# Kernel optimization log

Hardware: AMD Instinct MI355X
Metric: run time of the kernel (lower is better)

Reference implementation:

```python
import jax, jax.numpy as jnp
import numpy as np

EMB = 768
HEADS = 8

def setup_inputs() -> dict:
    key = jax.random.key(0)
    ks = jax.random.split(key, 9)
    B, N, E = 16, 1024, EMB
    s = 1.0 / np.sqrt(E)
    x = jax.random.normal(ks[0], (B, N, E), dtype=jnp.float32)
    Wq = jax.random.normal(ks[1], (E, E), dtype=jnp.float32) * s
    bq = jnp.zeros((E,), dtype=jnp.float32)
    Wk = jax.random.normal(ks[2], (E, E), dtype=jnp.float32) * s
    bk = jnp.zeros((E,), dtype=jnp.float32)
    Wv = jax.random.normal(ks[3], (E, E), dtype=jnp.float32) * s
    bv = jnp.zeros((E,), dtype=jnp.float32)
    Wo = jax.random.normal(ks[4], (E, E), dtype=jnp.float32) * s
    bo = jnp.zeros((E,), dtype=jnp.float32)
    return {"x": x, "Wq": Wq, "bq": bq, "Wk": Wk, "bk": bk, "Wv": Wv, "bv": bv, "Wo": Wo, "bo": bo}

def reference(x, Wq, bq, Wk, bk, Wv, bv, Wo, bo):
    B, N, E = x.shape
    H = HEADS
    D = E // H
    # separate Q/K/V linears, split heads: b n (h d) -> b h n d
    q = (x @ Wq + bq).reshape(B, N, H, D).transpose(0, 2, 1, 3)
    k = (x @ Wk + bk).reshape(B, N, H, D).transpose(0, 2, 1, 3)
    v = (x @ Wv + bv).reshape(B, N, H, D).transpose(0, 2, 1, 3)
    energy = jnp.einsum('bhqd,bhkd->bhqk', q, k)
    # NON-STANDARD: softmax first, then divide by sqrt(emb_size)
    scaling = jnp.float32(E) ** 0.5
    attn = jax.nn.softmax(energy, axis=-1) / scaling
    out = jnp.einsum('bhqk,bhkd->bhqd', attn, v)
    out = out.transpose(0, 2, 1, 3).reshape(B, N, E)  # b h n d -> b n (h d)
    return out @ Wo + bo
```

## Files before the change

### kernel.cpp

```cpp
#include <hip/hip_runtime.h>


typedef _Float16 half8 __attribute__((ext_vector_type(8)));
typedef __fp16 fp16x2 __attribute__((ext_vector_type(2)));
typedef float f32x4 __attribute__((ext_vector_type(4)));
typedef float f32x16 __attribute__((ext_vector_type(16)));

__device__ __forceinline__ void gload_lds16(const void* g, void* l) {
  __builtin_amdgcn_global_load_lds((const __attribute__((address_space(1))) void*)g,
                                   (__attribute__((address_space(3))) void*)l, 16, 0, 0);
}


__global__ __launch_bounds__(256) void conv_x_kernel(const float* __restrict__ x,
                                                     _Float16* __restrict__ xh) {
  long i = ((long)blockIdx.x * 256 + threadIdx.x) * 8;
  float4 a = *(const float4*)(x + i);
  float4 b = *(const float4*)(x + i + 4);
  half8 o;
  o[0] = (_Float16)a.x; o[1] = (_Float16)a.y; o[2] = (_Float16)a.z; o[3] = (_Float16)a.w;
  o[4] = (_Float16)b.x; o[5] = (_Float16)b.y; o[6] = (_Float16)b.z; o[7] = (_Float16)b.w;
  *(half8*)(xh + i) = o;
}

__global__ __launch_bounds__(256) void transpose_cvt_kernel(
    const float* __restrict__ W0, const float* __restrict__ W1,
    const float* __restrict__ W2, const float* __restrict__ W3,
    _Float16* __restrict__ WT) {
  __shared__ float tile[32][33];
  int z = blockIdx.z;
  const float* W = (z == 0) ? W0 : (z == 1) ? W1 : (z == 2) ? W2 : W3;
  int k0 = blockIdx.y * 32, n0 = blockIdx.x * 32;
  int tx = threadIdx.x, ty = threadIdx.y;
#pragma unroll
  for (int j = ty; j < 32; j += 8)
    tile[j][tx] = W[(size_t)(k0 + j) * 768 + n0 + tx];
  __syncthreads();
  _Float16* dst = WT + (size_t)z * 768 * 768;
#pragma unroll
  for (int j = ty; j < 32; j += 8)
    dst[(size_t)(n0 + j) * 768 + k0 + tx] = (_Float16)tile[tx][j];
}

__global__ __launch_bounds__(256) void conv_bias_kernel(const float* __restrict__ bq,
                                                        const float* __restrict__ bk,
                                                        const float* __restrict__ bv,
                                                        float* __restrict__ bias) {
  int i = blockIdx.x * 256 + threadIdx.x;
  if (i >= 2304) return;
  bias[i] = (i < 768) ? bq[i] : (i < 1536) ? bk[i - 768] : bv[i - 1536];
}


template <int OUT_F16>
__global__ __launch_bounds__(512, 2) void gemm256_kernel(
    const _Float16* __restrict__ A, const _Float16* __restrict__ Bt,
    const float* __restrict__ bias, void* __restrict__ C,
    int M, int N, int K, int ldc) {
  __shared__ _Float16 As[2][256 * 64];
  __shared__ _Float16 Bs[2][256 * 64];
  int nbx = N >> 8;
  int nwg = gridDim.x, wg = blockIdx.x;
  int cpx = nwg >> 3;
  int swz = (wg & 7) * cpx + (wg >> 3);
  int bx = swz % nbx, by = swz / nbx;
  int m0 = by * 256, n0 = bx * 256;
  int t = threadIdx.x, l = t & 63, w = t >> 6;
  int lg = l >> 4, lr = l & 15;
  int wr = w >> 2, wc = w & 3;
  f32x4 acc[8][4] = {};

  int srow[4], ssc[4];
#pragma unroll
  for (int j = 0; j < 4; ++j) {
    int slot = j * 512 + t;
    srow[j] = slot >> 3;
    ssc[j] = ((slot & 7) ^ (srow[j] & 7)) * 8;
  }

  auto stage = [&](int kt, int bi) {
    int k0 = kt * 64;
#pragma unroll
    for (int j = 0; j < 4; ++j)
      gload_lds16(A + (size_t)(m0 + srow[j]) * K + k0 + ssc[j], &As[bi][(j * 512 + t) * 8]);
#pragma unroll
    for (int j = 0; j < 4; ++j)
      gload_lds16(Bt + (size_t)(n0 + srow[j]) * K + k0 + ssc[j], &Bs[bi][(j * 512 + t) * 8]);
  };

  auto compute = [&](int bi) {
#pragma unroll
    for (int kk = 0; kk < 2; ++kk) {
      half8 bf[4];
#pragma unroll
      for (int nf = 0; nf < 4; ++nf) {
        int row = wc * 64 + nf * 16 + lr;
        bf[nf] = *(const half8*)&Bs[bi][row * 64 + ((kk * 4 + lg) ^ (row & 7)) * 8];
      }
#pragma unroll
      for (int mf = 0; mf < 8; ++mf) {
        int row = wr * 128 + mf * 16 + lr;
        half8 af = *(const half8*)&As[bi][row * 64 + ((kk * 4 + lg) ^ (row & 7)) * 8];
#pragma unroll
        for (int nf = 0; nf < 4; ++nf)
          acc[mf][nf] = __builtin_amdgcn_mfma_f32_16x16x32_f16(af, bf[nf], acc[mf][nf], 0, 0, 0);
      }
    }
  };

  int nkt = K >> 6;
  stage(0, 0);
  for (int kt = 0; kt < nkt; ++kt) {
    int bi = kt & 1;
    if (kt + 1 < nkt) {
      stage(kt + 1, bi ^ 1);
      asm volatile("s_waitcnt vmcnt(8)" ::: "memory");
    } else {
      asm volatile("s_waitcnt vmcnt(0)" ::: "memory");
    }
    __builtin_amdgcn_sched_barrier(0);
    __builtin_amdgcn_s_barrier();
    __builtin_amdgcn_sched_barrier(0);
    compute(bi);
    __builtin_amdgcn_sched_barrier(0);
    __builtin_amdgcn_s_barrier();
  }

#pragma unroll
  for (int mf = 0; mf < 8; ++mf)
#pragma unroll
    for (int nf = 0; nf < 4; ++nf) {
      int col = n0 + wc * 64 + nf * 16 + lr;
      float bb = bias[col];
#pragma unroll
      for (int i = 0; i < 4; ++i) {
        int row = m0 + wr * 128 + mf * 16 + lg * 4 + i;
        float v = acc[mf][nf][i] + bb;
        if (OUT_F16)
          ((_Float16*)C)[(size_t)row * ldc + col] = (_Float16)v;
        else
          ((float*)C)[(size_t)row * ldc + col] = v;
      }
    }
}


__global__ __launch_bounds__(256, 2) void attn_kernel(const _Float16* __restrict__ QKV,
                                                      _Float16* __restrict__ Oh) {
  int hw = blockIdx.x;
  int lin = (hw & 7) * 128 + (hw >> 3);
  int bh = lin >> 3, qt = lin & 7;
  int b = bh >> 3, h = bh & 7;
  int t = threadIdx.x, w = t >> 6, l = t & 63;
  int lr = l & 31, hi = l >> 5;

  __shared__ __align__(16) char KF[2][12288];
  __shared__ __align__(16) _Float16 VF[2][96 * 64];

  const _Float16* Qb = QKV + (size_t)b * 1024 * 2304 + h * 96;
  const _Float16* Kb = Qb + 768;
  const _Float16* Vb = Qb + 1536;

  half8 qf[6];
  {
    int qrow = qt * 128 + w * 32 + lr;
    const _Float16 s = (_Float16)1.4426950408889634f;
#pragma unroll
    for (int c = 0; c < 6; ++c) {
      qf[c] = *(const half8*)&Qb[(size_t)qrow * 2304 + c * 16 + hi * 8];
#pragma unroll
      for (int e = 0; e < 8; ++e) qf[c][e] = qf[c][e] * s;
    }
  }

  int ks_src[3], ks_dst[3];
#pragma unroll
  for (int j = 0; j < 3; ++j) {
    int s = j * 256 + t;
    int f = s >> 6, lane = s & 63;
    int sb = f / 6, c = f - sb * 6;
    ks_src[j] = (sb * 32 + (lane & 31)) * 2304 + c * 16 + ((lane >> 5) & 1) * 8;
    ks_dst[j] = s * 16;
  }
  bool vact[2];
  int v_src[2], v_dst[2][8];
#pragma unroll
  for (int j = 0; j < 2; ++j) {
    int u = j * 256 + t;
    vact[j] = u < 384;
    int kvp = u / 12, mm = u % 12;
    v_src[j] = 2 * kvp * 2304 + mm * 8;
#pragma unroll
    for (int e = 0; e < 8; ++e) {
      int d = mm * 8 + e;
      int sw = ((d & 7) ^ ((d >> 3) & 7)) << 3;
      v_dst[j][e] = d * 64 + ((2 * kvp) ^ sw);
    }
  }

  auto stage = [&](int kv0, int bi) {
    size_t goff = (size_t)kv0 * 2304;
#pragma unroll
    for (int j = 0; j < 3; ++j)
      gload_lds16(Kb + goff + ks_src[j], &KF[bi][ks_dst[j]]);
#pragma unroll
    for (int j = 0; j < 2; ++j)
      if (vact[j]) {
        const _Float16* vp = Vb + goff + v_src[j];
        half8 v0 = *(const half8*)vp;
        half8 v1 = *(const half8*)(vp + 2304);
#pragma unroll
        for (int e = 0; e < 8; ++e) {
          union { _Float16 h2[2]; unsigned u32; } pk;
          pk.h2[0] = v0[e]; pk.h2[1] = v1[e];
          *(unsigned*)&VF[bi][v_dst[j][e]] = pk.u32;
        }
      }
  };

  float m_run = -3.0e38f, l_run = 0.f;
  f32x16 oa[3] = {};

  stage(0, 0);

  for (int tile = 0; tile < 16; ++tile) {
    int bi = tile & 1;
    __syncthreads();
    if (tile + 1 < 16) stage((tile + 1) * 64, bi ^ 1);

    f32x16 sA[2] = {};
#pragma unroll
    for (int sb = 0; sb < 2; ++sb)
#pragma unroll
      for (int c = 0; c < 6; ++c) {
        half8 kf = *(const half8*)(KF[bi] + (sb * 6 + c) * 1024 + l * 16);
        sA[sb] = __builtin_amdgcn_mfma_f32_32x32x16_f16(kf, qf[c], sA[sb], 0, 0, 0);
      }

    float tmax = -3.0e38f;
#pragma unroll
    for (int sb = 0; sb < 2; ++sb)
#pragma unroll
      for (int r = 0; r < 16; ++r) tmax = fmaxf(tmax, sA[sb][r]);
    tmax = fmaxf(tmax, __shfl_xor(tmax, 32, 64));

    if (!__all(tmax <= m_run + 11.5f)) {
      float m_new = fmaxf(m_run, tmax);
      float scale = __builtin_exp2f(m_run - m_new);
#pragma unroll
      for (int r = 0; r < 16; ++r) {
        float sr = __shfl(scale, (r & 3) + 8 * (r >> 2) + 4 * hi, 64);
        oa[0][r] *= sr; oa[1][r] *= sr; oa[2][r] *= sr;
      }
      l_run *= scale;
      m_run = m_new;
    }

    unsigned keep[8], send[8];
    float rs = 0.f;
#pragma unroll
    for (int sb = 0; sb < 2; ++sb) {
      float e[16];
#pragma unroll
      for (int r = 0; r < 16; ++r) {
        e[r] = __builtin_exp2f(sA[sb][r] - m_run);
        rs += e[r];
      }
      unsigned w32[8];
#pragma unroll
      for (int p = 0; p < 4; ++p)
#pragma unroll
        for (int m = 0; m < 2; ++m) {
          union { fp16x2 h2; unsigned u; } pk;
          pk.h2 = __builtin_amdgcn_cvt_pkrtz(e[4 * p + 2 * m], e[4 * p + 2 * m + 1]);
          w32[p * 2 + m] = pk.u;
        }
#pragma unroll
      for (int kb = 0; kb < 2; ++kb)
#pragma unroll
        for (int m = 0; m < 2; ++m) {
          keep[sb * 4 + kb * 2 + m] = hi ? w32[(2 * kb + 1) * 2 + m] : w32[(2 * kb) * 2 + m];
          send[sb * 4 + kb * 2 + m] = hi ? w32[(2 * kb) * 2 + m] : w32[(2 * kb + 1) * 2 + m];
        }
    }
    rs += __shfl_xor(rs, 32, 64);
    l_run += rs;

    unsigned recv[8];
#pragma unroll
    for (int i = 0; i < 8; ++i) recv[i] = __shfl_xor(send[i], 32, 64);

#pragma unroll
    for (int kstep = 0; kstep < 4; ++kstep) {
      int base = (kstep >> 1) * 4 + (kstep & 1) * 2;
      union { unsigned u[4]; half8 h8; } pa;
      pa.u[0] = hi ? recv[base + 0] : keep[base + 0];
      pa.u[1] = hi ? recv[base + 1] : keep[base + 1];
      pa.u[2] = hi ? keep[base + 0] : recv[base + 0];
      pa.u[3] = hi ? keep[base + 1] : recv[base + 1];
#pragma unroll
      for (int dt = 0; dt < 3; ++dt) {
        int d = dt * 32 + lr;
        int sw = ((d & 7) ^ ((d >> 3) & 7)) << 3;
        half8 vf = *(const half8*)&VF[bi][d * 64 + ((kstep * 16 + hi * 8) ^ sw)];
        oa[dt] = __builtin_amdgcn_mfma_f32_32x32x16_f16(pa.h8, vf, oa[dt], 0, 0, 0);
      }
    }
  }

  float inv = 1.0f / (l_run * 27.712812921102035f);
  size_t rbase = (size_t)(b * 1024 + qt * 128 + w * 32) * 768 + h * 96;
#pragma unroll
  for (int r = 0; r < 16; ++r) {
    int q = (r & 3) + 8 * (r >> 2) + 4 * hi;
    float ivr = __shfl(inv, q, 64);
#pragma unroll
    for (int dt = 0; dt < 3; ++dt)
      Oh[rbase + (size_t)q * 768 + dt * 32 + lr] = (_Float16)(oa[dt][r] * ivr);
  }
}


extern "C" void kernel_launch(void* const* d_in, const int* in_sizes, int n_in,
                              void* d_out, int out_size, void* d_ws, size_t ws_size,
                              hipStream_t stream) {
  const float* x  = (const float*)d_in[0];
  const float* Wq = (const float*)d_in[1];
  const float* bq = (const float*)d_in[2];
  const float* Wk = (const float*)d_in[3];
  const float* bk = (const float*)d_in[4];
  const float* Wv = (const float*)d_in[5];
  const float* bv = (const float*)d_in[6];
  const float* Wo = (const float*)d_in[7];
  const float* bo = (const float*)d_in[8];
  float* out = (float*)d_out;

  char* ws = (char*)d_ws;
  _Float16* WT   = (_Float16*)(ws);
  float*    bias = (float*)(ws + 4718592);
  _Float16* xh   = (_Float16*)(ws + 4751360);
  _Float16* QKV  = (_Float16*)(ws + 29917184);
  _Float16* Oh   = (_Float16*)(ws + 105414656);

  conv_x_kernel<<<6144, 256, 0, stream>>>(x, xh);
  transpose_cvt_kernel<<<dim3(24, 24, 4), dim3(32, 8), 0, stream>>>(Wq, Wk, Wv, Wo, WT);
  conv_bias_kernel<<<9, 256, 0, stream>>>(bq, bk, bv, bias);

  gemm256_kernel<1><<<576, 512, 0, stream>>>(xh, WT, bias, QKV, 16384, 2304, 768, 2304);

  attn_kernel<<<1024, 256, 0, stream>>>(QKV, Oh);

  gemm256_kernel<0><<<192, 512, 0, stream>>>(Oh, WT + (size_t)2304 * 768, bo, out,
                                             16384, 768, 768, 768);
}
```

Before: 235.4 us.

## Replace 256x256 pipelined GEMM with simpler 128x128 tile GEMM and raise attention occupancy

Replaces the double-buffered, swizzled 256x256 GEMM with a single-buffered 128x128 tile kernel using 32-wide K steps and two barriers per step, and launches more workgroups. The aim is better occupancy and load balance across CUs for the projection GEMMs. It gives up load/compute overlap and the LDS swizzle, so bank conflicts and more frequent synchronisation are likely. It also raises the attention kernel's occupancy hint from 2 to 3 waves per SIMD, which may cause register spills.

```diff
diff --git a/kernel.cpp b/kernel.cpp
--- a/kernel.cpp
+++ b/kernel.cpp
@@ -53,89 +53,59 @@
 
 
 template <int OUT_F16>
-__global__ __launch_bounds__(512, 2) void gemm256_kernel(
+__global__ __launch_bounds__(256) void gemm_nt_kernel(
     const _Float16* __restrict__ A, const _Float16* __restrict__ Bt,
     const float* __restrict__ bias, void* __restrict__ C,
     int M, int N, int K, int ldc) {
-  __shared__ _Float16 As[2][256 * 64];
-  __shared__ _Float16 Bs[2][256 * 64];
-  int nbx = N >> 8;
-  int nwg = gridDim.x, wg = blockIdx.x;
+  __shared__ _Float16 As[128 * 32];
+  __shared__ _Float16 Bs[128 * 32];
+  int nbx = N >> 7;
+  int nwg = gridDim.x;
+  int wg = blockIdx.x;
   int cpx = nwg >> 3;
   int swz = (wg & 7) * cpx + (wg >> 3);
   int bx = swz % nbx, by = swz / nbx;
-  int m0 = by * 256, n0 = bx * 256;
+  int m0 = by * 128, n0 = bx * 128;
   int t = threadIdx.x, l = t & 63, w = t >> 6;
   int lg = l >> 4, lr = l & 15;
-  int wr = w >> 2, wc = w & 3;
-  f32x4 acc[8][4] = {};
-
-  int srow[4], ssc[4];
-#pragma unroll
-  for (int j = 0; j < 4; ++j) {
-    int slot = j * 512 + t;
-    srow[j] = slot >> 3;
-    ssc[j] = ((slot & 7) ^ (srow[j] & 7)) * 8;
-  }
-
-  auto stage = [&](int kt, int bi) {
-    int k0 = kt * 64;
-#pragma unroll
-    for (int j = 0; j < 4; ++j)
-      gload_lds16(A + (size_t)(m0 + srow[j]) * K + k0 + ssc[j], &As[bi][(j * 512 + t) * 8]);
-#pragma unroll
-    for (int j = 0; j < 4; ++j)
-      gload_lds16(Bt + (size_t)(n0 + srow[j]) * K + k0 + ssc[j], &Bs[bi][(j * 512 + t) * 8]);
-  };
-
-  auto compute = [&](int bi) {
-#pragma unroll
-    for (int kk = 0; kk < 2; ++kk) {
-      half8 bf[4];
-#pragma unroll
-      for (int nf = 0; nf < 4; ++nf) {
-        int row = wc * 64 + nf * 16 + lr;
-        bf[nf] = *(const half8*)&Bs[bi][row * 64 + ((kk * 4 + lg) ^ (row & 7)) * 8];
-      }
-#pragma unroll
-      for (int mf = 0; mf < 8; ++mf) {
-        int row = wr * 128 + mf * 16 + lr;
-        half8 af = *(const half8*)&As[bi][row * 64 + ((kk * 4 + lg) ^ (row & 7)) * 8];
-#pragma unroll
-        for (int nf = 0; nf < 4; ++nf)
-          acc[mf][nf] = __builtin_amdgcn_mfma_f32_16x16x32_f16(af, bf[nf], acc[mf][nf], 0, 0, 0);
-      }
-    }
-  };
-
-  int nkt = K >> 6;
-  stage(0, 0);
-  for (int kt = 0; kt < nkt; ++kt) {
-    int bi = kt & 1;
-    if (kt + 1 < nkt) {
-      stage(kt + 1, bi ^ 1);
-      asm volatile("s_waitcnt vmcnt(8)" ::: "memory");
-    } else {
-      asm volatile("s_waitcnt vmcnt(0)" ::: "memory");
-    }
-    __builtin_amdgcn_sched_barrier(0);
-    __builtin_amdgcn_s_barrier();
-    __builtin_amdgcn_sched_barrier(0);
-    compute(bi);
-    __builtin_amdgcn_sched_barrier(0);
-    __builtin_amdgcn_s_barrier();
-  }
-
-#pragma unroll
-  for (int mf = 0; mf < 8; ++mf)
-#pragma unroll
-    for (int nf = 0; nf < 4; ++nf) {
-      int col = n0 + wc * 64 + nf * 16 + lr;
+  int wr = w >> 1, wc = w & 1;
+  f32x4 acc[4][4] = {};
+
+  for (int k0 = 0; k0 < K; k0 += 32) {
+    __syncthreads();
+#pragma unroll
+    for (int j = 0; j < 2; ++j) {
+      int slot = j * 256 + t;
+      gload_lds16(A + (size_t)(m0 + (slot >> 2)) * K + k0 + (slot & 3) * 8, &As[slot * 8]);
+    }
+#pragma unroll
+    for (int j = 0; j < 2; ++j) {
+      int slot = j * 256 + t;
+      gload_lds16(Bt + (size_t)(n0 + (slot >> 2)) * K + k0 + (slot & 3) * 8, &Bs[slot * 8]);
+    }
+    __syncthreads();
+    half8 af[4], bf[4];
+#pragma unroll
+    for (int r = 0; r < 4; ++r) af[r] = *(const half8*)&As[(wr * 64 + r * 16 + lr) * 32 + lg * 8];
+#pragma unroll
+    for (int c = 0; c < 4; ++c) bf[c] = *(const half8*)&Bs[(wc * 64 + c * 16 + lr) * 32 + lg * 8];
+#pragma unroll
+    for (int r = 0; r < 4; ++r)
+#pragma unroll
+      for (int c = 0; c < 4; ++c)
+        acc[r][c] = __builtin_amdgcn_mfma_f32_16x16x32_f16(af[r], bf[c], acc[r][c], 0, 0, 0);
+  }
+
+#pragma unroll
+  for (int r = 0; r < 4; ++r)
+#pragma unroll
+    for (int c = 0; c < 4; ++c) {
+      int col = n0 + wc * 64 + c * 16 + lr;
       float bb = bias[col];
 #pragma unroll
       for (int i = 0; i < 4; ++i) {
-        int row = m0 + wr * 128 + mf * 16 + lg * 4 + i;
-        float v = acc[mf][nf][i] + bb;
+        int row = m0 + wr * 64 + r * 16 + lg * 4 + i;
+        float v = acc[r][c][i] + bb;
         if (OUT_F16)
           ((_Float16*)C)[(size_t)row * ldc + col] = (_Float16)v;
         else
@@ -145,7 +115,7 @@
 }
 
 
-__global__ __launch_bounds__(256, 2) void attn_kernel(const _Float16* __restrict__ QKV,
+__global__ __launch_bounds__(256, 3) void attn_kernel(const _Float16* __restrict__ QKV,
                                                       _Float16* __restrict__ Oh) {
   int hw = blockIdx.x;
   int lin = (hw & 7) * 128 + (hw >> 3);
@@ -346,10 +316,10 @@
   transpose_cvt_kernel<<<dim3(24, 24, 4), dim3(32, 8), 0, stream>>>(Wq, Wk, Wv, Wo, WT);
   conv_bias_kernel<<<9, 256, 0, stream>>>(bq, bk, bv, bias);
 
-  gemm256_kernel<1><<<576, 512, 0, stream>>>(xh, WT, bias, QKV, 16384, 2304, 768, 2304);
+  gemm_nt_kernel<1><<<2304, 256, 0, stream>>>(xh, WT, bias, QKV, 16384, 2304, 768, 2304);
 
   attn_kernel<<<1024, 256, 0, stream>>>(QKV, Oh);
 
-  gemm256_kernel<0><<<192, 512, 0, stream>>>(Oh, WT + (size_t)2304 * 768, bo, out,
+  gemm_nt_kernel<0><<<768, 256, 0, stream>>>(Oh, WT + (size_t)2304 * 768, bo, out,
                                              16384, 768, 768, 768);
 }
```

Result: no change. 238.8 us (+1.4%).
